# Optimization experiments

Measured on AMD Instinct MI355X. Metric: run time of the kernel, lower is better.

The kernel has to match this reference:

```python
import jax, jax.numpy as jnp
import numpy as np

HID = 256
HEADS = 8
HEAD_DIM = HID // HEADS
B, S = 2, 2048
EPS = 1e-5
NEG = -1e9


def _layernorm(x, g, b):
    m = jnp.mean(x, axis=-1, keepdims=True)
    v = jnp.mean(jnp.square(x - m), axis=-1, keepdims=True)
    return (x - m) / jnp.sqrt(v + EPS) * g + b


def setup_inputs() -> dict:
    key = jax.random.key(0)
    ks = jax.random.split(key, 12)
    x = jax.random.normal(ks[0], (B, S, HID), dtype=jnp.float32)
    adj_mask = jax.random.bernoulli(ks[1], 0.05, (B, S, S))
    sc = 0.02
    inp = {
        "x": x,
        "adj_mask": adj_mask,
        "ln1_g": jnp.ones((HID,), jnp.float32),
        "ln1_b": jnp.zeros((HID,), jnp.float32),
        "ln2_g": jnp.ones((HID,), jnp.float32),
        "ln2_b": jnp.zeros((HID,), jnp.float32),
        "Wq": sc * jax.random.normal(ks[2], (HID, HID), jnp.float32),
        "bq": jnp.zeros((HID,), jnp.float32),
        "Wk": sc * jax.random.normal(ks[3], (HID, HID), jnp.float32),
        "bk": jnp.zeros((HID,), jnp.float32),
        "Wv": sc * jax.random.normal(ks[4], (HID, HID), jnp.float32),
        "bv": jnp.zeros((HID,), jnp.float32),
        "Wo": sc * jax.random.normal(ks[5], (HID, HID), jnp.float32),
        "bo": jnp.zeros((HID,), jnp.float32),
        "W1": sc * jax.random.normal(ks[6], (HID, 4 * HID), jnp.float32),
        "b1": jnp.zeros((4 * HID,), jnp.float32),
        "W2": sc * jax.random.normal(ks[7], (4 * HID, HID), jnp.float32),
        "b2": jnp.zeros((HID,), jnp.float32),
    }
    return inp


def reference(x, adj_mask, ln1_g, ln1_b, ln2_g, ln2_b,
              Wq, bq, Wk, bk, Wv, bv, Wo, bo, W1, b1, W2, b2):
    b, s, _ = x.shape
    residual = x
    nx = _layernorm(x, ln1_g, ln1_b)
    # projections; weights stored as (in, out)
    q = (nx @ Wq + bq).reshape(b, s, HEADS, HEAD_DIM).transpose(0, 2, 1, 3)
    k = (nx @ Wk + bk).reshape(b, s, HEADS, HEAD_DIM).transpose(0, 2, 1, 3)
    v = (nx @ Wv + bv).reshape(b, s, HEADS, HEAD_DIM).transpose(0, 2, 1, 3)
    scores = jnp.einsum("bhqd,bhkd->bhqk", q, k) / jnp.sqrt(
        jnp.asarray(HEAD_DIM, x.dtype))
    scores = jnp.where(adj_mask[:, None, :, :], scores,
                       jnp.asarray(NEG, scores.dtype))
    attn = jax.nn.softmax(scores, axis=-1)
    out = jnp.einsum("bhqk,bhkd->bhqd", attn, v)
    out = out.transpose(0, 2, 1, 3).reshape(b, s, HID)
    out = out @ Wo + bo
    x = residual + out
    residual = x
    nx2 = _layernorm(x, ln2_g, ln2_b)
    h = jax.nn.gelu(nx2 @ W1 + b1, approximate=False)  # torch nn.GELU default is exact
    mlp = h @ W2 + b2
    return residual + mlp
```

## Files before the change

### kernel.cpp

```cpp
#include <hip/hip_runtime.h>
#include <hip/hip_bf16.h>

#define HID 256
#define HEADS 8
#define HDIM 32
#define BATCH 2
#define SEQ 2048
#define MROWS (BATCH*SEQ)
#define SCALE 0.17677669529663687f

typedef __attribute__((ext_vector_type(8))) short short8;
typedef __attribute__((ext_vector_type(4))) float f32x4;
typedef __attribute__((ext_vector_type(4))) unsigned uint4v;

static __device__ __forceinline__ unsigned short f2bf(float x) {
    __hip_bfloat16 h = __float2bfloat16(x);
    return __builtin_bit_cast(unsigned short, h);
}
static __device__ __forceinline__ unsigned cvtpk(float lo, float hi) {
    unsigned r;
    asm("v_cvt_pk_bf16_f32 %0, %1, %2" : "=v"(r) : "v"(lo), "v"(hi));
    return r;
}

__global__ __launch_bounds__(256) void detect_mask(const unsigned* __restrict__ m,
                                                   unsigned* __restrict__ flag)
{
    unsigned bad = 0;
    for (size_t i = (size_t)blockIdx.x * 256 + threadIdx.x; i < 262144u;
         i += (size_t)gridDim.x * 256) {
        const unsigned wv = m[i];
        if (wv != 0u && wv != 1u && wv != 0x3F800000u) bad = 1;
    }
    if (__ballot(bad)) {
        if ((threadIdx.x & 63) == 0) atomicOr(flag, 1u);
    }
}

__global__ __launch_bounds__(256) void tconv_all(
    const float* __restrict__ Wq, const float* __restrict__ Wk,
    const float* __restrict__ Wv, const float* __restrict__ Wo,
    const float* __restrict__ W1, const float* __restrict__ W2,
    __hip_bfloat16* __restrict__ Wtqkv, __hip_bfloat16* __restrict__ Wto,
    __hip_bfloat16* __restrict__ Wt1,   __hip_bfloat16* __restrict__ Wt2)
{
    const int t = blockIdx.x;
    const float* W; __hip_bfloat16* Wt; int K, N, tt;
    if      (t < 64)  { W = Wq; Wt = Wtqkv;          K = 256;  N = 256;  tt = t; }
    else if (t < 128) { W = Wk; Wt = Wtqkv + 65536;  K = 256;  N = 256;  tt = t - 64; }
    else if (t < 192) { W = Wv; Wt = Wtqkv + 131072; K = 256;  N = 256;  tt = t - 128; }
    else if (t < 256) { W = Wo; Wt = Wto;            K = 256;  N = 256;  tt = t - 192; }
    else if (t < 512) { W = W1; Wt = Wt1;            K = 256;  N = 1024; tt = t - 256; }
    else              { W = W2; Wt = Wt2;            K = 1024; N = 256;  tt = t - 512; }
    const int nt = N >> 5;
    const int n0 = (tt % nt) * 32, k0 = (tt / nt) * 32;
    __shared__ float tle[32][33];
    const int tx = threadIdx.x & 31, ty = threadIdx.x >> 5;
#pragma unroll
    for (int i = 0; i < 4; ++i)
        tle[ty + i*8][tx] = W[(size_t)(k0 + ty + i*8) * N + n0 + tx];
    __syncthreads();
#pragma unroll
    for (int i = 0; i < 4; ++i)
        Wt[(size_t)(n0 + ty + i*8) * K + k0 + tx] = __float2bfloat16(tle[tx][ty + i*8]);
}

__global__ __launch_bounds__(256) void ln_wave(const float* __restrict__ in,
                                               const float* __restrict__ g,
                                               const float* __restrict__ b,
                                               __hip_bfloat16* __restrict__ out)
{
    const int wave = threadIdx.x >> 6, lane = threadIdx.x & 63;
    const int row = blockIdx.x * 4 + wave;
    const float4 v = ((const float4*)(in + ((size_t)row << 8)))[lane];
    float s = v.x + v.y + v.z + v.w;
    for (int o = 32; o; o >>= 1) s += __shfl_xor(s, o);
    const float m = s * (1.f/HID);
    const float4 dv = make_float4(v.x - m, v.y - m, v.z - m, v.w - m);
    float vs = dv.x*dv.x + dv.y*dv.y + dv.z*dv.z + dv.w*dv.w;
    for (int o = 32; o; o >>= 1) vs += __shfl_xor(vs, o);
    const float rstd = rsqrtf(vs * (1.f/HID) + 1e-5f);
    const float4 gv = ((const float4*)g)[lane];
    const float4 bv = ((const float4*)b)[lane];
    ushort4 o4;
    o4.x = f2bf(dv.x * rstd * gv.x + bv.x);
    o4.y = f2bf(dv.y * rstd * gv.y + bv.y);
    o4.z = f2bf(dv.z * rstd * gv.z + bv.z);
    o4.w = f2bf(dv.w * rstd * gv.w + bv.w);
    ((ushort4*)(out + ((size_t)row << 8)))[lane] = o4;
}

__global__ __launch_bounds__(256) void gemm_qkv(const __hip_bfloat16* __restrict__ A,
                                                const __hip_bfloat16* __restrict__ Wt,
                                                const float* __restrict__ bq,
                                                const float* __restrict__ bk,
                                                const float* __restrict__ bv,
                                                __hip_bfloat16* __restrict__ qh,
                                                __hip_bfloat16* __restrict__ kh,
                                                __hip_bfloat16* __restrict__ vt)
{
    const int tid = threadIdx.x;
    const int wv = tid >> 6, lane = tid & 63;
    const int wr = wv >> 1, wc = wv & 1;
    const int r0 = blockIdx.x * 64 + wr * 32;
    const int c0 = blockIdx.y * 64 + wc * 32;
    const int al = lane & 15, ah = lane >> 4;

    f32x4 acc[2][2] = {};
    const short8* Ap[2];
    const short8* Bp[2];
#pragma unroll
    for (int m = 0; m < 2; ++m)
        Ap[m] = (const short8*)(A + (size_t)(r0 + m*16 + al) * 256 + ah * 8);
#pragma unroll
    for (int n = 0; n < 2; ++n)
        Bp[n] = (const short8*)(Wt + (size_t)(c0 + n*16 + al) * 256 + ah * 8);

#pragma unroll 8
    for (int kt = 0; kt < 8; ++kt) {
        short8 af[2], bf[2];
#pragma unroll
        for (int m = 0; m < 2; ++m) af[m] = Ap[m][kt*4];
#pragma unroll
        for (int n = 0; n < 2; ++n) bf[n] = Bp[n][kt*4];
#pragma unroll
        for (int m = 0; m < 2; ++m)
#pragma unroll
            for (int n = 0; n < 2; ++n)
                acc[m][n] = __builtin_amdgcn_mfma_f32_16x16x32_bf16(
                    af[m], bf[n], acc[m][n], 0, 0, 0);
    }

#pragma unroll
    for (int m = 0; m < 2; ++m)
#pragma unroll
        for (int n = 0; n < 2; ++n) {
            const int col = c0 + n*16 + al;
            const int which = col >> 8, cc = col & 255;
            const int h = cc >> 5, d = cc & 31;
            const float* bp = which == 0 ? bq : (which == 1 ? bk : bv);
            const float bvv = bp[cc];
            const int row0 = r0 + m*16 + ah*4;
            const int bb = row0 >> 11, s0 = row0 & 2047;
            if (which == 2) {
                ushort4 o4;
                o4.x = f2bf(acc[m][n][0] + bvv);
                o4.y = f2bf(acc[m][n][1] + bvv);
                o4.z = f2bf(acc[m][n][2] + bvv);
                o4.w = f2bf(acc[m][n][3] + bvv);
                *(ushort4*)(vt + ((size_t)((bb*8 + h)*32 + d) << 11) + s0) = o4;
            } else {
                __hip_bfloat16* op = which == 0 ? qh : kh;
                const float sc = which == 0 ? SCALE : 1.f;
#pragma unroll
                for (int r = 0; r < 4; ++r) {
                    const float v = (acc[m][n][r] + bvv) * sc;
                    op[(((size_t)(bb*8 + h) << 11) + s0 + r) * 32 + d] =
                        __float2bfloat16(v);
                }
            }
        }
}

__global__ __launch_bounds__(256) void attn_part(const __hip_bfloat16* __restrict__ Qh,
                                                 const __hip_bfloat16* __restrict__ Kh,
                                                 const __hip_bfloat16* __restrict__ Vt,
                                                 const void* __restrict__ mask,
                                                 const unsigned* __restrict__ flag,
                                                 float* __restrict__ part_o,
                                                 float* __restrict__ part_l)
{
    const int wave = threadIdx.x >> 6, lane = threadIdx.x & 63;
    const int wid = blockIdx.x * 4 + wave;
    const int tile = wid >> 2, ks = wid & 3;
    const int bh = tile >> 7, qt = tile & 127;
    const int b = bh >> 3;
    const int q0 = qt << 4;
    const int qi = lane & 15, g = lane >> 4;
    const int bytemode = (*flag != 0);
    const int kbeg = ks << 9;

    const short8 qf = *(const short8*)(Qh + (((size_t)bh << 11) + q0 + qi) * 32 + g*8);

    const __hip_bfloat16* Kb = Kh + ((size_t)bh << 16);
    const __hip_bfloat16* Vb = Vt + ((size_t)bh << 16);
    const unsigned char* mb = (const unsigned char*)mask
                            + (((size_t)b << 11) + q0 + qi) * 2048;
    const unsigned* mw = (const unsigned*)mask
                       + (((size_t)b << 11) + q0 + qi) * 2048;

    const int slA = ((2*g) & 3) * 16 + qi;
    const int slB = ((2*g + 1) & 3) * 16 + qi;
    const bool hi = g >= 2;

    f32x4 o0 = {}, o1 = {};
    const f32x4 zero = {};
    float lsum = 0.f;

    for (int k0 = kbeg; k0 < kbeg + 512; k0 += 32) {
        const short8 kf0 = *(const short8*)(Kb + ((size_t)(k0      + qi) << 5) + g*8);
        const short8 kf1 = *(const short8*)(Kb + ((size_t)(k0 + 16 + qi) << 5) + g*8);
        const short8 vf0 = *(const short8*)(Vb + ((size_t) qi       << 11) + k0 + g*8);
        const short8 vf1 = *(const short8*)(Vb + ((size_t)(qi + 16) << 11) + k0 + g*8);

        f32x4 s0 = __builtin_amdgcn_mfma_f32_16x16x32_bf16(kf0, qf, zero, 0, 0, 0);
        f32x4 s1 = __builtin_amdgcn_mfma_f32_16x16x32_bf16(kf1, qf, zero, 0, 0, 0);

        float p0[4], p1[4];
        if (bytemode) {
            const unsigned m0 = *(const unsigned*)(mb + k0 + 4*g);
            const unsigned m1 = *(const unsigned*)(mb + k0 + 16 + 4*g);
#pragma unroll
            for (int r = 0; r < 4; ++r) {
                p0[r] = ((m0 >> (8*r)) & 255u) ? __expf(s0[r]) : 0.f;
                p1[r] = ((m1 >> (8*r)) & 255u) ? __expf(s1[r]) : 0.f;
            }
        } else {
            const uint4v m0 = *(const uint4v*)(mw + k0 + 4*g);
            const uint4v m1 = *(const uint4v*)(mw + k0 + 16 + 4*g);
#pragma unroll
            for (int r = 0; r < 4; ++r) {
                p0[r] = m0[r] ? __expf(s0[r]) : 0.f;
                p1[r] = m1[r] ? __expf(s1[r]) : 0.f;
            }
        }
        lsum += ((p0[0] + p0[1]) + (p0[2] + p0[3]))
              + ((p1[0] + p1[1]) + (p1[2] + p1[3]));

        const unsigned f0w0 = cvtpk(p0[0], p0[1]), f0w1 = cvtpk(p0[2], p0[3]);
        const unsigned f1w0 = cvtpk(p1[0], p1[1]), f1w1 = cvtpk(p1[2], p1[3]);

        const unsigned aw0 = __shfl(f0w0, slA), aw1 = __shfl(f0w1, slA);
        const unsigned aw2 = __shfl(f0w0, slB), aw3 = __shfl(f0w1, slB);
        const unsigned cw0 = __shfl(f1w0, slA), cw1 = __shfl(f1w1, slA);
        const unsigned cw2 = __shfl(f1w0, slB), cw3 = __shfl(f1w1, slB);
        uint4v pw;
        pw[0] = hi ? cw0 : aw0;
        pw[1] = hi ? cw1 : aw1;
        pw[2] = hi ? cw2 : aw2;
        pw[3] = hi ? cw3 : aw3;
        const short8 pb = __builtin_bit_cast(short8, pw);

        o0 = __builtin_amdgcn_mfma_f32_16x16x32_bf16(vf0, pb, o0, 0, 0, 0);
        o1 = __builtin_amdgcn_mfma_f32_16x16x32_bf16(vf1, pb, o1, 0, 0, 0);
    }

    lsum += __shfl_xor(lsum, 16);
    lsum += __shfl_xor(lsum, 32);

    float* po = part_o + ((size_t)wid << 9) + qi*32 + 4*g;
    *(f32x4*)(po)      = o0;
    *(f32x4*)(po + 16) = o1;
    if (g == 0) part_l[(wid << 4) + qi] = lsum;
}

__global__ __launch_bounds__(256) void attn_comb(const float* __restrict__ part_o,
                                                 const float* __restrict__ part_l,
                                                 __hip_bfloat16* __restrict__ out)
{
    const int e = blockIdx.x * 256 + threadIdx.x;
    const int tile = e >> 9, j = e & 511;
    const int q = j >> 5, d = j & 31;
    float a = 0.f, l = 0.f;
#pragma unroll
    for (int s = 0; s < 4; ++s) {
        a += part_o[((size_t)(tile*4 + s) << 9) + j];
        l += part_l[((tile*4 + s) << 4) + q];
    }
    const int bh = tile >> 7, qt = tile & 127;
    const int b = bh >> 3, h = bh & 7;
    out[(((size_t)b << 11) + qt*16 + q) * 256 + h*32 + d] = __float2bfloat16(a / l);
}

template<int KTOT, int EPI>
__global__ __launch_bounds__(256) void gemm_mfma(const __hip_bfloat16* __restrict__ A,
                                                 const __hip_bfloat16* __restrict__ Wt,
                                                 const float* __restrict__ bias,
                                                 const float* __restrict__ res,
                                                 float* __restrict__ outF,
                                                 __hip_bfloat16* __restrict__ outB,
                                                 int N)
{
    const int tid = threadIdx.x;
    const int wv = tid >> 6, lane = tid & 63;
    const int wr = wv >> 1, wc = wv & 1;
    const int r0 = blockIdx.x * 64 + wr * 32;
    const int c0 = blockIdx.y * 64 + wc * 32;
    const int al = lane & 15, ah = lane >> 4;

    f32x4 acc[2][2] = {};
    const short8* Ap[2];
    const short8* Bp[2];
#pragma unroll
    for (int m = 0; m < 2; ++m)
        Ap[m] = (const short8*)(A + (size_t)(r0 + m*16 + al) * KTOT + ah * 8);
#pragma unroll
    for (int n = 0; n < 2; ++n)
        Bp[n] = (const short8*)(Wt + (size_t)(c0 + n*16 + al) * KTOT + ah * 8);

#pragma unroll 8
    for (int kt = 0; kt < KTOT/32; ++kt) {
        short8 af[2], bf[2];
#pragma unroll
        for (int m = 0; m < 2; ++m) af[m] = Ap[m][kt*4];
#pragma unroll
        for (int n = 0; n < 2; ++n) bf[n] = Bp[n][kt*4];
#pragma unroll
        for (int m = 0; m < 2; ++m)
#pragma unroll
            for (int n = 0; n < 2; ++n)
                acc[m][n] = __builtin_amdgcn_mfma_f32_16x16x32_bf16(
                    af[m], bf[n], acc[m][n], 0, 0, 0);
    }

#pragma unroll
    for (int m = 0; m < 2; ++m)
#pragma unroll
        for (int n = 0; n < 2; ++n) {
            const int col = c0 + n*16 + al;
            const float bv = bias[col];
#pragma unroll
            for (int r = 0; r < 4; ++r) {
                const int row = r0 + m*16 + ah*4 + r;
                const float v = acc[m][n][r] + bv;
                const size_t o = (size_t)row * N + col;
                if (EPI == 1) {
                    outF[o] = v + res[o];
                } else {
                    outB[o] = __float2bfloat16(
                        0.5f * v * (1.0f + erff(v * 0.70710678118654752f)));
                }
            }
        }
}

template<int KTOT>
__global__ __launch_bounds__(512) void gemm_ks(const __hip_bfloat16* __restrict__ A,
                                               const __hip_bfloat16* __restrict__ Wt,
                                               const float* __restrict__ bias,
                                               const float* __restrict__ res,
                                               float* __restrict__ outF,
                                               int N)
{
    constexpr int KH = KTOT / 2;
    __shared__ float red[4][64][17];
    const int tid = threadIdx.x;
    const int wv = tid >> 6, lane = tid & 63;
    const int t = wv & 3, ks = wv >> 2;
    const int wr = t >> 1, wc = t & 1;
    const int r0 = blockIdx.x * 64 + wr * 32;
    const int c0 = blockIdx.y * 64 + wc * 32;
    const int al = lane & 15, ah = lane >> 4;

    f32x4 acc[2][2] = {};
    const short8* Ap[2];
    const short8* Bp[2];
#pragma unroll
    for (int m = 0; m < 2; ++m)
        Ap[m] = (const short8*)(A + (size_t)(r0 + m*16 + al) * KTOT + ks*KH + ah * 8);
#pragma unroll
    for (int n = 0; n < 2; ++n)
        Bp[n] = (const short8*)(Wt + (size_t)(c0 + n*16 + al) * KTOT + ks*KH + ah * 8);

#pragma unroll 8
    for (int kt = 0; kt < KH/32; ++kt) {
        short8 af[2], bf[2];
#pragma unroll
        for (int m = 0; m < 2; ++m) af[m] = Ap[m][kt*4];
#pragma unroll
        for (int n = 0; n < 2; ++n) bf[n] = Bp[n][kt*4];
#pragma unroll
        for (int m = 0; m < 2; ++m)
#pragma unroll
            for (int n = 0; n < 2; ++n)
                acc[m][n] = __builtin_amdgcn_mfma_f32_16x16x32_bf16(
                    af[m], bf[n], acc[m][n], 0, 0, 0);
    }

    if (ks == 1) {
#pragma unroll
        for (int m = 0; m < 2; ++m)
#pragma unroll
            for (int n = 0; n < 2; ++n)
#pragma unroll
                for (int r = 0; r < 4; ++r)
                    red[t][lane][(m*2 + n)*4 + r] = acc[m][n][r];
    }
    __syncthreads();
    if (ks == 0) {
#pragma unroll
        for (int m = 0; m < 2; ++m)
#pragma unroll
            for (int n = 0; n < 2; ++n) {
                const int col = c0 + n*16 + al;
                const float bv = bias[col];
#pragma unroll
                for (int r = 0; r < 4; ++r) {
                    const int row = r0 + m*16 + ah*4 + r;
                    const float v = acc[m][n][r] + red[t][lane][(m*2 + n)*4 + r] + bv;
                    const size_t o = (size_t)row * N + col;
                    outF[o] = v + res[o];
                }
            }
    }
}

extern "C" void kernel_launch(void* const* d_in, const int* in_sizes, int n_in,
                              void* d_out, int out_size, void* d_ws, size_t ws_size,
                              hipStream_t stream)
{
    const float* x    = (const float*)d_in[0];
    const void*  mask = d_in[1];
    const float* ln1g = (const float*)d_in[2];
    const float* ln1b = (const float*)d_in[3];
    const float* ln2g = (const float*)d_in[4];
    const float* ln2b = (const float*)d_in[5];
    const float* Wq   = (const float*)d_in[6];
    const float* bq   = (const float*)d_in[7];
    const float* Wk   = (const float*)d_in[8];
    const float* bk   = (const float*)d_in[9];
    const float* Wv   = (const float*)d_in[10];
    const float* bv   = (const float*)d_in[11];
    const float* Wo   = (const float*)d_in[12];
    const float* bo   = (const float*)d_in[13];
    const float* W1   = (const float*)d_in[14];
    const float* b1   = (const float*)d_in[15];
    const float* W2   = (const float*)d_in[16];
    const float* b2   = (const float*)d_in[17];

    char* w = (char*)d_ws;
    unsigned* flag        = (unsigned*)(w);
    __hip_bfloat16* qh    = (__hip_bfloat16*)(w + 4096);
    __hip_bfloat16* kh    = qh  + (size_t)MROWS * HID;
    __hip_bfloat16* vt    = kh  + (size_t)MROWS * HID;
    __hip_bfloat16* nx    = vt  + (size_t)MROWS * HID;
    __hip_bfloat16* attn_b= nx  + (size_t)MROWS * HID;
    __hip_bfloat16* nx2   = attn_b + (size_t)MROWS * HID;
    __hip_bfloat16* hbuf  = nx2 + (size_t)MROWS * HID;
    float* x1             = (float*)(hbuf + (size_t)MROWS * 4*HID);
    __hip_bfloat16* Wtqkv = (__hip_bfloat16*)(x1 + (size_t)MROWS * HID);
    __hip_bfloat16* Wto   = Wtqkv + 196608;
    __hip_bfloat16* Wt1   = Wto + 65536;
    __hip_bfloat16* Wt2   = Wt1 + 262144;
    float* part_o         = (float*)(Wt2 + 262144);
    float* part_l         = part_o + (size_t)8192 * 512;
    float* ob   = (float*)d_out;

    hipMemsetAsync(flag, 0, 4, stream);
    detect_mask<<<128, 256, 0, stream>>>((const unsigned*)mask, flag);
    tconv_all<<<768, 256, 0, stream>>>(Wq, Wk, Wv, Wo, W1, W2, Wtqkv, Wto, Wt1, Wt2);
    ln_wave<<<MROWS/4, 256, 0, stream>>>(x, ln1g, ln1b, nx);
    gemm_qkv<<<dim3(64,12), 256, 0, stream>>>(nx, Wtqkv, bq, bk, bv, qh, kh, vt);
    attn_part<<<2048, 256, 0, stream>>>(qh, kh, vt, mask, flag, part_o, part_l);
    attn_comb<<<4096, 256, 0, stream>>>(part_o, part_l, attn_b);
    gemm_ks<256><<<dim3(64,4), 512, 0, stream>>>(attn_b, Wto, bo, x, x1, HID);
    ln_wave<<<MROWS/4, 256, 0, stream>>>(x1, ln2g, ln2b, nx2);
    gemm_mfma<256,2><<<dim3(64,16), 256, 0, stream>>>(nx2, Wt1, b1, nullptr, nullptr, hbuf, 4*HID);
    gemm_ks<1024><<<dim3(64,4), 512, 0, stream>>>(hbuf, Wt2, b2, x1, ob, HID);
}
```

Measured before the change: 259.5 us.

## Pack adjacency mask into bitmask once and halve attention key splits

Adds a pack_mask kernel that turns the byte or word adjacency mask into a 1-bit-per-key bitmask, so that the attention kernel reads one 32-bit word per 32 keys and no longer reads the full mask once per head. The attention split-K is reduced from 4 to 2 partitions, each covering 1024 keys, which halves the partial-output traffic and makes the combine kernel cheaper. The cost is an extra kernel launch that reads the full mask, and fewer waves in the attention kernel, which could reduce latency hiding.

Measured after the change: 241.5 us. 1.07x faster.

```diff
diff --git a/kernel.cpp b/kernel.cpp
--- a/kernel.cpp
+++ b/kernel.cpp
@@ -35,6 +35,24 @@
     if (__ballot(bad)) {
         if ((threadIdx.x & 63) == 0) atomicOr(flag, 1u);
     }
+}
+
+__global__ __launch_bounds__(256) void pack_mask(const void* __restrict__ mask,
+                                                 const unsigned* __restrict__ flag,
+                                                 unsigned char* __restrict__ bm)
+{
+    const int row = blockIdx.x, t = threadIdx.x;
+    unsigned byte = 0;
+    if (*flag != 0) {
+        const unsigned char* src = (const unsigned char*)mask + ((size_t)row << 11) + t*8;
+#pragma unroll
+        for (int i = 0; i < 8; ++i) byte |= (unsigned)(src[i] != 0) << i;
+    } else {
+        const unsigned* src = (const unsigned*)mask + ((size_t)row << 11) + t*8;
+#pragma unroll
+        for (int i = 0; i < 8; ++i) byte |= (unsigned)(src[i] != 0u) << i;
+    }
+    bm[((size_t)row << 8) + t] = (unsigned char)byte;
 }
 
 __global__ __launch_bounds__(256) void tconv_all(
@@ -165,29 +183,24 @@
 __global__ __launch_bounds__(256) void attn_part(const __hip_bfloat16* __restrict__ Qh,
                                                  const __hip_bfloat16* __restrict__ Kh,
                                                  const __hip_bfloat16* __restrict__ Vt,
-                                                 const void* __restrict__ mask,
-                                                 const unsigned* __restrict__ flag,
+                                                 const unsigned* __restrict__ bm32,
                                                  float* __restrict__ part_o,
                                                  float* __restrict__ part_l)
 {
     const int wave = threadIdx.x >> 6, lane = threadIdx.x & 63;
     const int wid = blockIdx.x * 4 + wave;
-    const int tile = wid >> 2, ks = wid & 3;
+    const int tile = wid >> 1, ks = wid & 1;
     const int bh = tile >> 7, qt = tile & 127;
     const int b = bh >> 3;
     const int q0 = qt << 4;
     const int qi = lane & 15, g = lane >> 4;
-    const int bytemode = (*flag != 0);
-    const int kbeg = ks << 9;
+    const int kbeg = ks << 10;
 
     const short8 qf = *(const short8*)(Qh + (((size_t)bh << 11) + q0 + qi) * 32 + g*8);
 
     const __hip_bfloat16* Kb = Kh + ((size_t)bh << 16);
     const __hip_bfloat16* Vb = Vt + ((size_t)bh << 16);
-    const unsigned char* mb = (const unsigned char*)mask
-                            + (((size_t)b << 11) + q0 + qi) * 2048;
-    const unsigned* mw = (const unsigned*)mask
-                       + (((size_t)b << 11) + q0 + qi) * 2048;
+    const unsigned* mrow = bm32 + (((size_t)(b << 11) + q0 + qi) << 6);
 
     const int slA = ((2*g) & 3) * 16 + qi;
     const int slB = ((2*g + 1) & 3) * 16 + qi;
@@ -197,7 +210,8 @@
     const f32x4 zero = {};
     float lsum = 0.f;
 
-    for (int k0 = kbeg; k0 < kbeg + 512; k0 += 32) {
+    for (int k0 = kbeg; k0 < kbeg + 1024; k0 += 32) {
+        const unsigned mwrd = mrow[k0 >> 5];
         const short8 kf0 = *(const short8*)(Kb + ((size_t)(k0      + qi) << 5) + g*8);
         const short8 kf1 = *(const short8*)(Kb + ((size_t)(k0 + 16 + qi) << 5) + g*8);
         const short8 vf0 = *(const short8*)(Vb + ((size_t) qi       << 11) + k0 + g*8);
@@ -207,22 +221,10 @@
         f32x4 s1 = __builtin_amdgcn_mfma_f32_16x16x32_bf16(kf1, qf, zero, 0, 0, 0);
 
         float p0[4], p1[4];
-        if (bytemode) {
-            const unsigned m0 = *(const unsigned*)(mb + k0 + 4*g);
-            const unsigned m1 = *(const unsigned*)(mb + k0 + 16 + 4*g);
-#pragma unroll
-            for (int r = 0; r < 4; ++r) {
-                p0[r] = ((m0 >> (8*r)) & 255u) ? __expf(s0[r]) : 0.f;
-                p1[r] = ((m1 >> (8*r)) & 255u) ? __expf(s1[r]) : 0.f;
-            }
-        } else {
-            const uint4v m0 = *(const uint4v*)(mw + k0 + 4*g);
-            const uint4v m1 = *(const uint4v*)(mw + k0 + 16 + 4*g);
-#pragma unroll
-            for (int r = 0; r < 4; ++r) {
-                p0[r] = m0[r] ? __expf(s0[r]) : 0.f;
-                p1[r] = m1[r] ? __expf(s1[r]) : 0.f;
-            }
+#pragma unroll
+        for (int r = 0; r < 4; ++r) {
+            p0[r] = ((mwrd >> (     4*g + r)) & 1u) ? __expf(s0[r]) : 0.f;
+            p1[r] = ((mwrd >> (16 + 4*g + r)) & 1u) ? __expf(s1[r]) : 0.f;
         }
         lsum += ((p0[0] + p0[1]) + (p0[2] + p0[3]))
               + ((p1[0] + p1[1]) + (p1[2] + p1[3]));
@@ -261,12 +263,9 @@
     const int e = blockIdx.x * 256 + threadIdx.x;
     const int tile = e >> 9, j = e & 511;
     const int q = j >> 5, d = j & 31;
-    float a = 0.f, l = 0.f;
-#pragma unroll
-    for (int s = 0; s < 4; ++s) {
-        a += part_o[((size_t)(tile*4 + s) << 9) + j];
-        l += part_l[((tile*4 + s) << 4) + q];
-    }
+    const float a = part_o[((size_t)(tile*2) << 9) + j]
+                  + part_o[((size_t)(tile*2+1) << 9) + j];
+    const float l = part_l[((tile*2) << 4) + q] + part_l[((tile*2+1) << 4) + q];
     const int bh = tile >> 7, qt = tile & 127;
     const int b = bh >> 3, h = bh & 7;
     out[(((size_t)b << 11) + qt*16 + q) * 256 + h*32 + d] = __float2bfloat16(a / l);
@@ -430,7 +429,8 @@
 
     char* w = (char*)d_ws;
     unsigned* flag        = (unsigned*)(w);
-    __hip_bfloat16* qh    = (__hip_bfloat16*)(w + 4096);
+    unsigned char* bmask  = (unsigned char*)(w + 4096);
+    __hip_bfloat16* qh    = (__hip_bfloat16*)(w + 4096 + (1 << 20));
     __hip_bfloat16* kh    = qh  + (size_t)MROWS * HID;
     __hip_bfloat16* vt    = kh  + (size_t)MROWS * HID;
     __hip_bfloat16* nx    = vt  + (size_t)MROWS * HID;
@@ -443,15 +443,17 @@
     __hip_bfloat16* Wt1   = Wto + 65536;
     __hip_bfloat16* Wt2   = Wt1 + 262144;
     float* part_o         = (float*)(Wt2 + 262144);
-    float* part_l         = part_o + (size_t)8192 * 512;
+    float* part_l         = part_o + (size_t)4096 * 512;
     float* ob   = (float*)d_out;
 
     hipMemsetAsync(flag, 0, 4, stream);
     detect_mask<<<128, 256, 0, stream>>>((const unsigned*)mask, flag);
+    pack_mask<<<MROWS, 256, 0, stream>>>(mask, flag, bmask);
     tconv_all<<<768, 256, 0, stream>>>(Wq, Wk, Wv, Wo, W1, W2, Wtqkv, Wto, Wt1, Wt2);
     ln_wave<<<MROWS/4, 256, 0, stream>>>(x, ln1g, ln1b, nx);
     gemm_qkv<<<dim3(64,12), 256, 0, stream>>>(nx, Wtqkv, bq, bk, bv, qh, kh, vt);
-    attn_part<<<2048, 256, 0, stream>>>(qh, kh, vt, mask, flag, part_o, part_l);
+    attn_part<<<1024, 256, 0, stream>>>(qh, kh, vt, (const unsigned*)bmask,
+                                        part_o, part_l);
     attn_comb<<<4096, 256, 0, stream>>>(part_o, part_l, attn_b);
     gemm_ks<256><<<dim3(64,4), 512, 0, stream>>>(attn_b, Wto, bo, x, x1, HID);
     ln_wave<<<MROWS/4, 256, 0, stream>>>(x1, ln2g, ln2b, nx2);
```
